# Optimization experiments

Hardware: AMD Instinct MI355X
Metric: run time of the kernel (lower is better)

Reference implementation:

```python
import jax, jax.numpy as jnp
import numpy as np

B, T, S, H, V = 4, 512, 1024, 768, 50257

def setup_inputs() -> dict:
    key = jax.random.key(0)
    k1, k2, k3, k4, k5, k6 = jax.random.split(key, 6)
    input_ids_to_copy = jax.random.randint(k1, (B, S), 0, V)
    cross_attentions = jax.random.uniform(k2, (B, T, S), dtype=jnp.float32)
    # normalize like attention weights
    cross_attentions = cross_attentions / jnp.sum(cross_attentions, axis=-1, keepdims=True)
    src_hidden_states = jax.random.normal(k3, (B, S, H), dtype=jnp.float32)
    tgt_hidden_states = jax.random.normal(k4, (B, T, H), dtype=jnp.float32)
    # p_gen_head = Linear(2H, 1) + Sigmoid
    W_pgen = jax.random.normal(k5, (2 * H, 1), dtype=jnp.float32) * (1.0 / np.sqrt(2 * H))
    b_pgen = jnp.zeros((1,), dtype=jnp.float32)
    return {
        "input_ids_to_copy": input_ids_to_copy,
        "cross_attentions": cross_attentions,
        "src_hidden_states": src_hidden_states,
        "tgt_hidden_states": tgt_hidden_states,
        "W_pgen": W_pgen,
        "b_pgen": b_pgen,
    }

def _copy_logits(attn_bts, ids_bs, vocab_size):
    # logits[b,t,v] = sum_s attn[b,t,s] * (ids[b,s] == v)
    # Efficient scatter-add over source positions instead of one-hot + matmul.
    def per_batch(attn_ts, ids_s):
        # attn_ts: [T,S], ids_s: [S] -> segment_sum over S -> [V,T] -> [T,V]
        return jax.ops.segment_sum(attn_ts.T, ids_s, num_segments=vocab_size).T
    return jax.vmap(per_batch)(attn_bts, ids_bs)

def reference(input_ids_to_copy, cross_attentions, src_hidden_states,
              tgt_hidden_states, W_pgen, b_pgen):
    # context_vectors: [B,T,H]
    context_vectors = jnp.einsum('bts,bsh->bth', cross_attentions, src_hidden_states)
    total_states = jnp.concatenate((context_vectors, tgt_hidden_states), axis=-1)  # [B,T,2H]
    p_gen = jax.nn.sigmoid(total_states @ W_pgen + b_pgen)  # [B,T,1]
    logits = _copy_logits(cross_attentions, input_ids_to_copy, V)  # [B,T,V]
    return (p_gen, logits)
```

## Files before the change

### kernel.cpp

```cpp
#include <hip/hip_runtime.h>
#include <math.h>

#define BB 4
#define TT 512
#define SS 1024
#define HH 768
#define VV 50257
#define NW 1571
#define NPROJ 1536
#define NROWS (BB * TT)
#define NV (NROWS * VV)
#define NG4 (NV / 4)
#define MEMB 2048
#define MSTRIDE (MEMB * 256)

__global__ __launch_bounds__(256) void prep_kernel(
    const float* __restrict__ src, const float* __restrict__ tgt,
    const float* __restrict__ W, const float* __restrict__ bptr,
    const int* __restrict__ ids,
    float* __restrict__ src_proj, float* __restrict__ tgt_proj,
    unsigned short* __restrict__ rank_g, float* __restrict__ out)
{
    __shared__ unsigned bm[NW];
    __shared__ unsigned pre[NW];
    __shared__ unsigned scan[256];
    const int tid = threadIdx.x;

    if (blockIdx.x >= NPROJ + BB) {
        float4* zp = (float4*)(out + NROWS);
        const float4 z4 = make_float4(0.f, 0.f, 0.f, 0.f);
        for (int g = (blockIdx.x - (NPROJ + BB)) * 256 + tid; g < NG4;
             g += MSTRIDE)
            zp[g] = z4;
        return;
    }

    if (blockIdx.x < NPROJ) {
        const int wave = tid >> 6;
        const int lane = tid & 63;
        const int row  = blockIdx.x * 4 + wave;

        const float* vec;
        const float* w;
        if (row < BB * SS) { vec = src + (size_t)row * HH;            w = W; }
        else               { vec = tgt + (size_t)(row - BB*SS) * HH;  w = W + HH; }
        const float4* v4 = (const float4*)vec;
        const float4* w4 = (const float4*)w;

        float acc = 0.f;
#pragma unroll
        for (int k = 0; k < 3; ++k) {
            float4 a = v4[k * 64 + lane];
            float4 b = w4[k * 64 + lane];
            acc += a.x * b.x + a.y * b.y + a.z * b.z + a.w * b.w;
        }
#pragma unroll
        for (int off = 32; off > 0; off >>= 1) acc += __shfl_down(acc, off);
        if (lane == 0) {
            if (row < BB * SS) src_proj[row] = acc;
            else               tgt_proj[row - BB * SS] = acc + bptr[0];
        }
        return;
    }

    const int b = blockIdx.x - NPROJ;

    for (int i = tid; i < NW; i += 256) bm[i] = 0u;
    __syncthreads();
    const int* idb = ids + b * SS;
    for (int s = tid; s < SS; s += 256) {
        const int v = idb[s];
        atomicOr(&bm[v >> 5], 1u << (v & 31));
    }
    __syncthreads();

    unsigned cnt[7];
    unsigned local = 0;
    const int w0 = tid * 7;
#pragma unroll
    for (int k = 0; k < 7; ++k) {
        const int w = w0 + k;
        cnt[k] = local;
        local += (w < NW) ? (unsigned)__popc(bm[w]) : 0u;
    }
    scan[tid] = local;
    __syncthreads();
    for (int off = 1; off < 256; off <<= 1) {
        const unsigned mine = scan[tid];
        const unsigned add  = (tid >= off) ? scan[tid - off] : 0u;
        __syncthreads();
        scan[tid] = mine + add;
        __syncthreads();
    }
    const unsigned excl = (tid > 0) ? scan[tid - 1] : 0u;
#pragma unroll
    for (int k = 0; k < 7; ++k) {
        const int w = w0 + k;
        if (w < NW) pre[w] = excl + cnt[k];
    }
    __syncthreads();
    for (int s = tid; s < SS; s += 256) {
        const int v = idb[s];
        const unsigned w = (unsigned)v >> 5, bit = (unsigned)v & 31u;
        const unsigned r = pre[w] + (unsigned)__popc(bm[w] & ((1u << bit) - 1u));
        rank_g[b * SS + s] = (unsigned short)r;
    }
}

__global__ __launch_bounds__(256) void row_kernel(
    const float* __restrict__ attn,
    const float* __restrict__ src_proj,
    const float* __restrict__ tgt_proj,
    const unsigned short* __restrict__ rank_g,
    const int* __restrict__ ids,
    float* __restrict__ out)
{
    __shared__ float vals[SS];
    __shared__ float wsum[4];

    const int row = blockIdx.x;
    const int b   = row >> 9;
    const int tid = threadIdx.x;

    ((float4*)vals)[tid] = make_float4(0.f, 0.f, 0.f, 0.f);
    __syncthreads();

    const float4  a = ((const float4*)(attn + (size_t)row * SS))[tid];
    const float4  p = ((const float4*)(src_proj + b * SS))[tid];
    const ushort4 r = ((const ushort4*)(rank_g + b * SS))[tid];
    atomicAdd(&vals[r.x], a.x);
    atomicAdd(&vals[r.y], a.y);
    atomicAdd(&vals[r.z], a.z);
    atomicAdd(&vals[r.w], a.w);
    float acc = a.x * p.x + a.y * p.y + a.z * p.z + a.w * p.w;
#pragma unroll
    for (int off = 32; off > 0; off >>= 1) acc += __shfl_down(acc, off);
    if ((tid & 63) == 0) wsum[tid >> 6] = acc;
    __syncthreads();

    if (tid == 0) {
        const float x = wsum[0] + wsum[1] + wsum[2] + wsum[3] + tgt_proj[row];
        out[row] = 1.f / (1.f + expf(-x));
    }

    float* lp = out + NROWS + (size_t)row * VV;
    const int*            idb = ids    + b * SS;
    const unsigned short* rb  = rank_g + b * SS;
    for (int s = tid; s < SS; s += 256)
        lp[idb[s]] = vals[rb[s]];
}

extern "C" void kernel_launch(void* const* d_in, const int* in_sizes, int n_in,
                              void* d_out, int out_size, void* d_ws, size_t ws_size,
                              hipStream_t stream) {
    const int*   ids  = (const int*)d_in[0];
    const float* attn = (const float*)d_in[1];
    const float* src  = (const float*)d_in[2];
    const float* tgt  = (const float*)d_in[3];
    const float* W    = (const float*)d_in[4];
    const float* bp   = (const float*)d_in[5];

    float* out = (float*)d_out;

    float*          src_proj = (float*)d_ws;
    float*          tgt_proj = src_proj + BB * SS;
    unsigned short* rank_g   = (unsigned short*)(tgt_proj + BB * TT);

    prep_kernel<<<NPROJ + BB + MEMB, 256, 0, stream>>>(
        src, tgt, W, bp, ids, src_proj, tgt_proj, rank_g, out);
    row_kernel<<<NROWS, 256, 0, stream>>>(
        attn, src_proj, tgt_proj, rank_g, ids, out);
}
```

Measured before the change: 524.2 us.

## Zero logits with hipMemsetAsync and scatter only unique ids per row

The hand-written zero-fill blocks inside the prep kernel are replaced by a hipMemsetAsync over the roughly 400MB logits buffer. Prep now also writes a compacted list of unique token ids and their count per batch. The row kernel then scatters one value per unique id instead of one per source position, which removes redundant duplicate writes. The memset can no longer overlap with the projection and rank work, and it depends on how well the runtime fill kernel performs.

```diff
diff --git a/kernel.cpp b/kernel.cpp
--- a/kernel.cpp
+++ b/kernel.cpp
@@ -9,31 +9,20 @@
 #define NW 1571
 #define NPROJ 1536
 #define NROWS (BB * TT)
-#define NV (NROWS * VV)
-#define NG4 (NV / 4)
-#define MEMB 2048
-#define MSTRIDE (MEMB * 256)
+#define NV ((size_t)NROWS * VV)
 
 __global__ __launch_bounds__(256) void prep_kernel(
     const float* __restrict__ src, const float* __restrict__ tgt,
     const float* __restrict__ W, const float* __restrict__ bptr,
     const int* __restrict__ ids,
     float* __restrict__ src_proj, float* __restrict__ tgt_proj,
-    unsigned short* __restrict__ rank_g, float* __restrict__ out)
+    unsigned short* __restrict__ rank_g, unsigned short* __restrict__ uids_g,
+    int* __restrict__ nuniq_g)
 {
     __shared__ unsigned bm[NW];
     __shared__ unsigned pre[NW];
     __shared__ unsigned scan[256];
     const int tid = threadIdx.x;
-
-    if (blockIdx.x >= NPROJ + BB) {
-        float4* zp = (float4*)(out + NROWS);
-        const float4 z4 = make_float4(0.f, 0.f, 0.f, 0.f);
-        for (int g = (blockIdx.x - (NPROJ + BB)) * 256 + tid; g < NG4;
-             g += MSTRIDE)
-            zp[g] = z4;
-        return;
-    }
 
     if (blockIdx.x < NPROJ) {
         const int wave = tid >> 6;
@@ -98,12 +87,14 @@
         const int w = w0 + k;
         if (w < NW) pre[w] = excl + cnt[k];
     }
+    if (tid == 255) nuniq_g[b] = (int)scan[255];
     __syncthreads();
     for (int s = tid; s < SS; s += 256) {
         const int v = idb[s];
         const unsigned w = (unsigned)v >> 5, bit = (unsigned)v & 31u;
         const unsigned r = pre[w] + (unsigned)__popc(bm[w] & ((1u << bit) - 1u));
         rank_g[b * SS + s] = (unsigned short)r;
+        uids_g[b * SS + r] = (unsigned short)v;
     }
 }
 
@@ -112,7 +103,8 @@
     const float* __restrict__ src_proj,
     const float* __restrict__ tgt_proj,
     const unsigned short* __restrict__ rank_g,
-    const int* __restrict__ ids,
+    const unsigned short* __restrict__ uids_g,
+    const int* __restrict__ nuniq_g,
     float* __restrict__ out)
 {
     __shared__ float vals[SS];
@@ -144,10 +136,10 @@
     }
 
     float* lp = out + NROWS + (size_t)row * VV;
-    const int*            idb = ids    + b * SS;
-    const unsigned short* rb  = rank_g + b * SS;
-    for (int s = tid; s < SS; s += 256)
-        lp[idb[s]] = vals[rb[s]];
+    const int nuniq = nuniq_g[b];
+    const unsigned short* ub = uids_g + b * SS;
+    for (int j = tid; j < nuniq; j += 256)
+        lp[ub[j]] = vals[j];
 }
 
 extern "C" void kernel_launch(void* const* d_in, const int* in_sizes, int n_in,
@@ -165,9 +157,13 @@
     float*          src_proj = (float*)d_ws;
     float*          tgt_proj = src_proj + BB * SS;
     unsigned short* rank_g   = (unsigned short*)(tgt_proj + BB * TT);
+    unsigned short* uids_g   = rank_g + BB * SS;
+    int*            nuniq_g  = (int*)(uids_g + BB * SS);
 
-    prep_kernel<<<NPROJ + BB + MEMB, 256, 0, stream>>>(
-        src, tgt, W, bp, ids, src_proj, tgt_proj, rank_g, out);
+    hipMemsetAsync(out + NROWS, 0, NV * sizeof(float), stream);
+
+    prep_kernel<<<NPROJ + BB, 256, 0, stream>>>(
+        src, tgt, W, bp, ids, src_proj, tgt_proj, rank_g, uids_g, nuniq_g);
     row_kernel<<<NROWS, 256, 0, stream>>>(
-        attn, src_proj, tgt_proj, rank_g, ids, out);
+        attn, src_proj, tgt_proj, rank_g, uids_g, nuniq_g, out);
 }
```

Measured after the change: 519.7 us. No clear change (-0.9%).
